# Kernel tuning notes

Measured on AMD Instinct MI355X. Metric: run time of the kernel, lower is better.

## Reference

```python
import jax, jax.numpy as jnp
import numpy as np

TAU_MIN, TAU_MAX = 5.0, 50.0
BOOST = 3.2
DECO_RATE = 0.01

B, I, F, Q = 4096, 1024, 2048, 4

def setup_inputs() -> dict:
    key = jax.random.key(0)
    ks = jax.random.split(key, 12)
    return {
        "inputs": jax.random.normal(ks[0], (B, I), jnp.float32),
        "hidden_state": jax.random.normal(ks[1], (B, F), jnp.float32),
        "W_in": jax.random.normal(ks[2], (I, F), jnp.float32) / np.sqrt(I),
        "b_in": jnp.zeros((F,), jnp.float32),
        "amp_real": jax.random.normal(ks[3], (F, Q), jnp.float32) * 0.1,
        "amp_imag": jax.random.normal(ks[4], (F, Q), jnp.float32) * 0.1,
        "phase": jax.random.uniform(ks[5], (F, Q), jnp.float32, 0.0, 2 * np.pi),
        "primary": jax.random.normal(ks[6], (F, F), jnp.float32) / np.sqrt(F),
        "ent_mat": jax.random.normal(ks[7], (F, F), jnp.float32) / np.sqrt(F),
        "corr": jax.random.uniform(ks[8], (F,), jnp.float32, 0.0, 0.7),
        "W_tau": jax.random.uniform(ks[9], (F, F), jnp.float32, 0.0, 0.1) / np.sqrt(F),
        "b_tau": jnp.zeros((F,), jnp.float32),
        "W_dec": jax.random.uniform(ks[10], (F, F), jnp.float32, 0.0, 0.5) / np.sqrt(F),
        "b_dec": jnp.zeros((F,), jnp.float32),
        "time_step": 1,
    }

def reference(inputs, hidden_state, W_in, b_in, amp_real, amp_imag, phase,
              primary, ent_mat, corr, W_tau, b_tau, W_dec, b_dec, time_step):
    t = jnp.float32(time_step)
    batch = inputs.shape[0]
    feats = hidden_state.shape[1]

    # input projection: [B,I] @ [I,F]
    x_proj = inputs @ W_in + b_in

    # quantum superposition state (batch-independent, [F,Q] params)
    ph = phase + t * 0.1
    real_c = amp_real * jnp.cos(ph)          # [F,Q]
    imag_c = amp_imag * jnp.sin(ph)          # [F,Q]
    sup_r = real_c.sum(-1)                    # [F]
    sup_i = imag_c.sum(-1)                    # [F]
    prob_amp = real_c ** 2 + imag_c ** 2      # [F,Q]
    q_state = sup_r * jnp.exp(-sup_i ** 2)    # [F]
    q_state_b = jnp.broadcast_to(q_state, (batch, feats))
    prob_amp_b = jnp.broadcast_to(prob_amp, (batch,) + prob_amp.shape)

    # entangled recurrent connections: two F x F matmuls
    ent_rec = hidden_state @ primary + (hidden_state @ ent_mat) * corr

    # quantum time constants
    tau_raw = q_state_b @ W_tau + b_tau
    tau_q = (TAU_MIN + (TAU_MAX - TAU_MIN) * jax.nn.sigmoid(tau_raw)) / BOOST

    # decoherence gate
    deco = jax.nn.sigmoid(q_state_b @ W_dec + b_dec)
    coherent = jnp.exp(-DECO_RATE * t)

    classical = jnp.tanh(x_proj + ent_rec)
    quantum_act = q_state_b * deco * coherent
    combined = classical + quantum_act

    dx_dt = (-hidden_state + combined) / tau_q
    dt_q = 0.1 / BOOST
    new_hidden = hidden_state + dt_q * dx_dt

    # diagnostics
    d_amp = jnp.mean(prob_amp_b, axis=-1)          # [B,F]
    d_coh = coherent
    d_ent = jnp.mean(jnp.abs(ent_rec))
    d_dec = jnp.mean(deco)
    d_tau = jnp.mean(tau_q)
    return (new_hidden, d_amp, d_coh, d_ent, d_dec, d_tau)
```

## Files before the change

kernel.cpp:

```cpp
#include <hip/hip_runtime.h>
#include <hip/hip_bf16.h>

#define BD 4096
#define ID 1024
#define FD 2048

typedef __bf16 v8bf __attribute__((ext_vector_type(8)));
typedef float  v4f  __attribute__((ext_vector_type(4)));

struct alignas(8) bf4 { __hip_bfloat16 x, y, z, w; };

__device__ inline __hip_bfloat16 bf(float f) { return __float2bfloat16(f); }
__device__ inline float sig(float x) { return 1.f / (1.f + expf(-x)); }

__device__ inline void gload16(const __hip_bfloat16* g, __hip_bfloat16* l) {
  __builtin_amdgcn_global_load_lds(
      (const __attribute__((address_space(1))) void*)g,
      (__attribute__((address_space(3))) void*)l, 16, 0, 0);
}

#define MB_CAST  12288
#define MB_PREP  (MB_CAST + 8)
#define MB_TCW   (MB_PREP + 2048)
#define MB_TCM   (MB_TCW + 4096)
#define MB_MV    (MB_TCM + 256)

__global__ void k_mega(
    const float* __restrict__ inputs, const float* __restrict__ hidden,
    const float* __restrict__ W_in, const float* __restrict__ primary,
    const float* __restrict__ ent_mat, const float* __restrict__ corr,
    const float* __restrict__ W_tau, const float* __restrict__ W_dec,
    const float* __restrict__ ar, const float* __restrict__ ai,
    const float* __restrict__ ph, const int* __restrict__ tstep,
    __hip_bfloat16* __restrict__ inputs_bf, __hip_bfloat16* __restrict__ hidden_bf,
    __hip_bfloat16* __restrict__ WT, __hip_bfloat16* __restrict__ MT,
    float* __restrict__ qs, float* __restrict__ pamp,
    float* __restrict__ ptau, float* __restrict__ pdec) {
  __shared__ float tbuf[32][33];
  __shared__ float q[128];
  const int b = blockIdx.x, tid = threadIdx.x;

  if (b < MB_CAST) {
    int i = b * 256 + tid;
    const float* src = inputs; __hip_bfloat16* dst = inputs_bf;
    int n1 = BD * ID / 4;
    if (i >= n1) { i -= n1; src = hidden; dst = hidden_bf; }
    float4 v = ((const float4*)src)[i];
    bf4 o{bf(v.x), bf(v.y), bf(v.z), bf(v.w)};
    ((bf4*)dst)[i] = o;

  } else if (b < MB_PREP) {
    int j = (b - MB_CAST) * 256 + tid;
    float t = (float)tstep[0];
    float4 a = ((const float4*)ar)[j];
    float4 bb = ((const float4*)ai)[j];
    float4 p = ((const float4*)ph)[j];
    float sr = 0.f, si = 0.f, pm = 0.f;
#pragma unroll
    for (int k = 0; k < 4; k++) {
      float pk = (&p.x)[k] + 0.1f * t;
      float rc = (&a.x)[k] * cosf(pk), ic = (&bb.x)[k] * sinf(pk);
      sr += rc; si += ic; pm += rc * rc + ic * ic;
    }
    qs[j] = sr * expf(-si * si);
    pamp[j] = 0.25f * pm;

  } else if (b < MB_TCM) {
    int isM = (b >= MB_TCW);
    int b2 = b - (isM ? MB_TCW : MB_PREP);
    const float* src = isM ? primary : W_in;
    const float* src2 = ent_mat;
    __hip_bfloat16* dst = isM ? MT : WT;
    int C = FD, R = isM ? FD : ID;
    int tx = tid & 31, ty = tid >> 5;
    int x = (b2 & 63) * 32 + tx;
    int yb = (b2 >> 6) * 32;
    float cr = isM ? corr[x] : 0.f;
#pragma unroll
    for (int j = 0; j < 4; j++) {
      int y = yb + ty + j * 8;
      float v = src[(size_t)y * C + x];
      if (isM) v += src2[(size_t)y * C + x] * cr;
      tbuf[ty + j * 8][tx] = v;
    }
    __syncthreads();
#pragma unroll
    for (int j = 0; j < 4; j++) {
      int orow = (b2 & 63) * 32 + ty + j * 8;
      int ocol = yb + tx;
      dst[(size_t)orow * R + ocol] = bf(tbuf[tx][ty + j * 8]);
    }

  } else {
    int b2 = b - MB_TCM;
    int jb = b2 & 7, p = (b2 >> 3) & 15, z = b2 >> 7;
    int i0 = p * 128;
    if (tid < 128) {
      int i = i0 + tid;
      float t = (float)tstep[0];
      float4 a = ((const float4*)ar)[i];
      float4 bb = ((const float4*)ai)[i];
      float4 pp = ((const float4*)ph)[i];
      float sr = 0.f, si = 0.f;
#pragma unroll
      for (int k = 0; k < 4; k++) {
        float pk = (&pp.x)[k] + 0.1f * t;
        sr += (&a.x)[k] * cosf(pk);
        si += (&bb.x)[k] * sinf(pk);
      }
      q[tid] = sr * expf(-si * si);
    }
    __syncthreads();
    const float* W = z ? W_dec : W_tau;
    float* outp = z ? pdec : ptau;
    int j = jb * 256 + tid;
    float acc = 0.f;
#pragma unroll 8
    for (int i = 0; i < 128; i++)
      acc = fmaf(q[i], W[(size_t)(i0 + i) * FD + j], acc);
    outp[p * FD + j] = acc;
  }
}

__global__ void k_post(const float* __restrict__ ptau, const float* __restrict__ pdec,
                       const float* __restrict__ qs, const float* __restrict__ b_tau,
                       const float* __restrict__ b_dec, const int* tstep,
                       float* __restrict__ s_arr, float* __restrict__ qact,
                       float* __restrict__ tpart, float* __restrict__ dpart) {
  int j = blockIdx.x * 256 + threadIdx.x;
  float tr = b_tau[j], dr = b_dec[j];
#pragma unroll
  for (int p = 0; p < 16; p++) {
    tr += ptau[p * FD + j];
    dr += pdec[p * FD + j];
  }
  float t = (float)tstep[0];
  float coh = expf(-0.01f * t);
  float tq = (5.f + 45.f * sig(tr)) / 3.2f;
  s_arr[j] = 0.03125f / tq;
  float dec = sig(dr);
  qact[j] = qs[j] * dec * coh;
  float tsum = tq, dsum = dec;
  for (int off = 32; off; off >>= 1) {
    tsum += __shfl_down(tsum, off);
    dsum += __shfl_down(dsum, off);
  }
  __shared__ float rt[4], rd[4];
  int w = threadIdx.x >> 6;
  if ((threadIdx.x & 63) == 0) { rt[w] = tsum; rd[w] = dsum; }
  __syncthreads();
  if (threadIdx.x == 0) {
    tpart[blockIdx.x] = rt[0] + rt[1] + rt[2] + rt[3];
    dpart[blockIdx.x] = rd[0] + rd[1] + rd[2] + rd[3];
  }
}

__global__ __launch_bounds__(256, 4) void k_gemm2(
    const __hip_bfloat16* __restrict__ Ah,
    const __hip_bfloat16* __restrict__ MT,
    const __hip_bfloat16* __restrict__ Ax,
    const __hip_bfloat16* __restrict__ WT,
    __hip_bfloat16* __restrict__ ge, __hip_bfloat16* __restrict__ gx) {
  __shared__ alignas(16) __hip_bfloat16 As[2][128][32];
  __shared__ alignas(16) __hip_bfloat16 Bs[2][128][32];

  const int tid = threadIdx.x;
  const int l = tid & 63, w = tid >> 6;
  const int wr = w >> 1, wc = w & 1;
  const int row0 = blockIdx.x * 128, col0 = blockIdx.y * 128;
  const int bz = blockIdx.z;

  const __hip_bfloat16* A = bz ? Ax : Ah;
  const __hip_bfloat16* B = bz ? WT : MT;
  const int ld = bz ? ID : FD;
  const int nkt = bz ? 32 : 64;
  __hip_bfloat16* gout = bz ? gx : ge;

  v4f acc[4][4];
#pragma unroll
  for (int i = 0; i < 4; i++)
#pragma unroll
    for (int j = 0; j < 4; j++) acc[i][j] = (v4f)0.f;

  const int srow = l >> 2;
  const int scol = ((l & 3) ^ ((l >> 3) & 3)) * 8;
  const int rcol = ((l >> 4) ^ ((l >> 1) & 3)) * 8;

  auto stage = [&](int buf, int kt) {
    int k = kt * 32;
#pragma unroll
    for (int i = 0; i < 2; i++) {
      int rr = w * 32 + i * 16;
      gload16(A + (size_t)(row0 + rr + srow) * ld + k + scol, &As[buf][rr][0]);
      gload16(B + (size_t)(col0 + rr + srow) * ld + k + scol, &Bs[buf][rr][0]);
    }
  };
  auto compute = [&](int buf) {
    v8bf a[4], b[4];
#pragma unroll
    for (int mi = 0; mi < 4; mi++)
      a[mi] = *(const v8bf*)&As[buf][wr * 64 + mi * 16 + (l & 15)][rcol];
#pragma unroll
    for (int ni = 0; ni < 4; ni++)
      b[ni] = *(const v8bf*)&Bs[buf][wc * 64 + ni * 16 + (l & 15)][rcol];
#pragma unroll
    for (int mi = 0; mi < 4; mi++)
#pragma unroll
      for (int ni = 0; ni < 4; ni++)
        acc[mi][ni] = __builtin_amdgcn_mfma_f32_16x16x32_bf16(a[mi], b[ni], acc[mi][ni], 0, 0, 0);
  };

  stage(0, 0);
  __syncthreads();
  for (int kt = 0; kt < nkt; kt++) {
    if (kt + 1 < nkt) stage((kt + 1) & 1, kt + 1);
    compute(kt & 1);
    __syncthreads();
  }

#pragma unroll
  for (int ni = 0; ni < 4; ni++) {
    int gc = col0 + wc * 64 + ni * 16 + (l & 15);
#pragma unroll
    for (int mi = 0; mi < 4; mi++) {
      int gr0 = row0 + wr * 64 + mi * 16 + (l >> 4) * 4;
#pragma unroll
      for (int e = 0; e < 4; e++)
        gout[(size_t)(gr0 + e) * FD + gc] = bf(acc[mi][ni][e]);
    }
  }
}

__global__ __launch_bounds__(256) void k_comb(
    const __hip_bfloat16* __restrict__ ge, const __hip_bfloat16* __restrict__ gx,
    const __hip_bfloat16* __restrict__ hbf,
    const float* __restrict__ b_in, const float* __restrict__ s_arr,
    const float* __restrict__ qact, const float* __restrict__ pamp,
    float* __restrict__ entpart, float* __restrict__ out) {
  const int row = blockIdx.x;
  const size_t rb = (size_t)row * FD;
  float asum = 0.f;
#pragma unroll
  for (int half = 0; half < 2; half++) {
    const int c = half * 1024 + threadIdx.x * 4;
    const size_t base = rb + c;
    bf4 e0 = *(const bf4*)(ge + base);
    bf4 xx = *(const bf4*)(gx + base);
    bf4 hh = *(const bf4*)(hbf + base);
    float4 bi = *(const float4*)&b_in[c];
    float4 sj = *(const float4*)&s_arr[c];
    float4 qa = *(const float4*)&qact[c];
    float4 pm = *(const float4*)&pamp[c];
    float o[4];
#pragma unroll
    for (int j = 0; j < 4; j++) {
      float e = __bfloat162float((&e0.x)[j]);
      asum += fabsf(e);
      float g = e + __bfloat162float((&xx.x)[j]) + (&bi.x)[j];
      float comb = tanhf(g) + (&qa.x)[j];
      float h = __bfloat162float((&hh.x)[j]);
      o[j] = fmaf((&sj.x)[j], comb - h, h);
    }
    *(float4*)&out[base] = make_float4(o[0], o[1], o[2], o[3]);
    *(float4*)&out[(size_t)BD * FD + base] = pm;
  }

  for (int off = 32; off; off >>= 1) asum += __shfl_down(asum, off);
  __shared__ float red[4];
  if ((threadIdx.x & 63) == 0) red[threadIdx.x >> 6] = asum;
  __syncthreads();
  if (threadIdx.x == 0)
    entpart[row] = red[0] + red[1] + red[2] + red[3];
}

__global__ void k_fin(const float* __restrict__ entpart, const float* __restrict__ tpart,
                      const float* __restrict__ dpart, const int* tstep, float* out3) {
  float s = 0.f;
  for (int i = threadIdx.x; i < BD; i += 256) s += entpart[i];
  for (int off = 32; off; off >>= 1) s += __shfl_down(s, off);
  __shared__ float red[4];
  if ((threadIdx.x & 63) == 0) red[threadIdx.x >> 6] = s;
  __syncthreads();
  if (threadIdx.x == 0) {
    float tot = red[0] + red[1] + red[2] + red[3];
    float ts = 0.f, ds = 0.f;
#pragma unroll
    for (int i = 0; i < 8; i++) { ts += tpart[i]; ds += dpart[i]; }
    float t = (float)tstep[0];
    out3[0] = expf(-0.01f * t);
    out3[1] = tot / (float)((size_t)BD * FD);
    out3[2] = ds / (float)FD;
    out3[3] = ts / (float)FD;
  }
}

extern "C" void kernel_launch(void* const* d_in, const int* in_sizes, int n_in,
                              void* d_out, int out_size, void* d_ws, size_t ws_size,
                              hipStream_t stream) {
  const float* inputs  = (const float*)d_in[0];
  const float* hidden  = (const float*)d_in[1];
  const float* W_in    = (const float*)d_in[2];
  const float* b_in    = (const float*)d_in[3];
  const float* amp_r   = (const float*)d_in[4];
  const float* amp_i   = (const float*)d_in[5];
  const float* phase   = (const float*)d_in[6];
  const float* primary = (const float*)d_in[7];
  const float* ent_mat = (const float*)d_in[8];
  const float* corr    = (const float*)d_in[9];
  const float* W_tau   = (const float*)d_in[10];
  const float* b_tau   = (const float*)d_in[11];
  const float* W_dec   = (const float*)d_in[12];
  const float* b_dec   = (const float*)d_in[13];
  const int*   tstep   = (const int*)d_in[14];

  char* ws = (char*)d_ws;
  __hip_bfloat16* inputs_bf = (__hip_bfloat16*)(ws + 0);
  __hip_bfloat16* hidden_bf = (__hip_bfloat16*)(ws + 8388608);
  __hip_bfloat16* WT        = (__hip_bfloat16*)(ws + 25165824);
  __hip_bfloat16* MT        = (__hip_bfloat16*)(ws + 29360128);
  __hip_bfloat16* ge        = (__hip_bfloat16*)(ws + 37748736);
  __hip_bfloat16* gx        = (__hip_bfloat16*)(ws + 54525952);

  char* sb = ws + 71303168;
  float* qs      = (float*)(sb);
  float* pamp    = (float*)(sb + 8192);
  float* s_arr   = (float*)(sb + 2 * 8192);
  float* qact    = (float*)(sb + 3 * 8192);
  float* ptau    = (float*)(sb + 4 * 8192);
  float* pdec    = (float*)(sb + 4 * 8192 + 131072);
  float* entpart = (float*)(sb + 4 * 8192 + 262144);
  float* tpart   = (float*)(sb + 4 * 8192 + 278528);
  float* dpart   = (float*)(sb + 4 * 8192 + 278528 + 64);

  float* out = (float*)d_out;

  hipLaunchKernelGGL(k_mega, dim3(MB_MV), dim3(256), 0, stream,
                     inputs, hidden, W_in, primary, ent_mat, corr, W_tau, W_dec,
                     amp_r, amp_i, phase, tstep,
                     inputs_bf, hidden_bf, WT, MT, qs, pamp, ptau, pdec);
  hipLaunchKernelGGL(k_post, dim3(8), dim3(256), 0, stream,
                     ptau, pdec, qs, b_tau, b_dec, tstep, s_arr, qact, tpart, dpart);
  hipLaunchKernelGGL(k_gemm2, dim3(32, 16, 2), dim3(256), 0, stream,
                     hidden_bf, MT, inputs_bf, WT, ge, gx);
  hipLaunchKernelGGL(k_comb, dim3(4096), dim3(256), 0, stream,
                     ge, gx, hidden_bf, b_in, s_arr, qact, pamp, entpart, out);
  hipLaunchKernelGGL(k_fin, dim3(1), dim3(256), 0, stream,
                     entpart, tpart, dpart, tstep, out + (size_t)2 * BD * FD);
}
```

Baseline: 125.8 us.

## Rebalance GEMM split-K across z-slices, fold k_post into GEMM launch, fast tanh

The hidden-state GEMM (K=2048) is split 48/16 k-tiles so that the z=1 blocks compute a partial hidden product plus the input projection (K=1024), evening out the work per block. A third partial buffer g2 is added and summed in the combine kernel. The small k_post kernel is folded into the GEMM launch as extra z=2 blocks, which removes one launch and its serialization. tanhf is replaced by an exp/rcp approximation. The costs are an extra bf16 intermediate write and read plus extra rounding, and many z=2 blocks launch only to exit immediately.

```diff
diff --git a/kernel.cpp b/kernel.cpp
--- a/kernel.cpp
+++ b/kernel.cpp
@@ -12,6 +12,10 @@
 
 __device__ inline __hip_bfloat16 bf(float f) { return __float2bfloat16(f); }
 __device__ inline float sig(float x) { return 1.f / (1.f + expf(-x)); }
+__device__ inline float tanh_fast(float x) {
+  float e = __expf(2.f * x);
+  return 1.f - 2.f * __builtin_amdgcn_rcpf(e + 1.f);
+}
 
 __device__ inline void gload16(const __hip_bfloat16* g, __hip_bfloat16* l) {
   __builtin_amdgcn_global_load_lds(
@@ -122,59 +126,57 @@
   }
 }
 
-__global__ void k_post(const float* __restrict__ ptau, const float* __restrict__ pdec,
-                       const float* __restrict__ qs, const float* __restrict__ b_tau,
-                       const float* __restrict__ b_dec, const int* tstep,
-                       float* __restrict__ s_arr, float* __restrict__ qact,
-                       float* __restrict__ tpart, float* __restrict__ dpart) {
-  int j = blockIdx.x * 256 + threadIdx.x;
-  float tr = b_tau[j], dr = b_dec[j];
-#pragma unroll
-  for (int p = 0; p < 16; p++) {
-    tr += ptau[p * FD + j];
-    dr += pdec[p * FD + j];
-  }
-  float t = (float)tstep[0];
-  float coh = expf(-0.01f * t);
-  float tq = (5.f + 45.f * sig(tr)) / 3.2f;
-  s_arr[j] = 0.03125f / tq;
-  float dec = sig(dr);
-  qact[j] = qs[j] * dec * coh;
-  float tsum = tq, dsum = dec;
-  for (int off = 32; off; off >>= 1) {
-    tsum += __shfl_down(tsum, off);
-    dsum += __shfl_down(dsum, off);
-  }
-  __shared__ float rt[4], rd[4];
-  int w = threadIdx.x >> 6;
-  if ((threadIdx.x & 63) == 0) { rt[w] = tsum; rd[w] = dsum; }
-  __syncthreads();
-  if (threadIdx.x == 0) {
-    tpart[blockIdx.x] = rt[0] + rt[1] + rt[2] + rt[3];
-    dpart[blockIdx.x] = rd[0] + rd[1] + rd[2] + rd[3];
-  }
-}
-
-__global__ __launch_bounds__(256, 4) void k_gemm2(
+__global__ __launch_bounds__(256, 4) void k_gemm3(
     const __hip_bfloat16* __restrict__ Ah,
     const __hip_bfloat16* __restrict__ MT,
     const __hip_bfloat16* __restrict__ Ax,
     const __hip_bfloat16* __restrict__ WT,
-    __hip_bfloat16* __restrict__ ge, __hip_bfloat16* __restrict__ gx) {
+    const float* __restrict__ ptau, const float* __restrict__ pdec,
+    const float* __restrict__ qs, const float* __restrict__ b_tau,
+    const float* __restrict__ b_dec, const int* __restrict__ tstep,
+    float* __restrict__ s_arr, float* __restrict__ qact,
+    float* __restrict__ tpart, float* __restrict__ dpart,
+    __hip_bfloat16* __restrict__ ge, __hip_bfloat16* __restrict__ g2,
+    __hip_bfloat16* __restrict__ gx) {
   __shared__ alignas(16) __hip_bfloat16 As[2][128][32];
   __shared__ alignas(16) __hip_bfloat16 Bs[2][128][32];
+  __shared__ float rt[4], rd[4];
 
   const int tid = threadIdx.x;
+
+  if (blockIdx.z == 2) {
+    if (blockIdx.x != 0 || blockIdx.y >= 8) return;
+    int j = blockIdx.y * 256 + tid;
+    float tr = b_tau[j], dr = b_dec[j];
+#pragma unroll
+    for (int p = 0; p < 16; p++) {
+      tr += ptau[p * FD + j];
+      dr += pdec[p * FD + j];
+    }
+    float t = (float)tstep[0];
+    float coh = expf(-0.01f * t);
+    float tq = (5.f + 45.f * sig(tr)) / 3.2f;
+    s_arr[j] = 0.03125f / tq;
+    float dec = sig(dr);
+    qact[j] = qs[j] * dec * coh;
+    float tsum = tq, dsum = dec;
+    for (int off = 32; off; off >>= 1) {
+      tsum += __shfl_down(tsum, off);
+      dsum += __shfl_down(dsum, off);
+    }
+    int w = tid >> 6;
+    if ((tid & 63) == 0) { rt[w] = tsum; rd[w] = dsum; }
+    __syncthreads();
+    if (tid == 0) {
+      tpart[blockIdx.y] = rt[0] + rt[1] + rt[2] + rt[3];
+      dpart[blockIdx.y] = rd[0] + rd[1] + rd[2] + rd[3];
+    }
+    return;
+  }
+
   const int l = tid & 63, w = tid >> 6;
   const int wr = w >> 1, wc = w & 1;
   const int row0 = blockIdx.x * 128, col0 = blockIdx.y * 128;
-  const int bz = blockIdx.z;
-
-  const __hip_bfloat16* A = bz ? Ax : Ah;
-  const __hip_bfloat16* B = bz ? WT : MT;
-  const int ld = bz ? ID : FD;
-  const int nkt = bz ? 32 : 64;
-  __hip_bfloat16* gout = bz ? gx : ge;
 
   v4f acc[4][4];
 #pragma unroll
@@ -186,8 +188,8 @@
   const int scol = ((l & 3) ^ ((l >> 3) & 3)) * 8;
   const int rcol = ((l >> 4) ^ ((l >> 1) & 3)) * 8;
 
-  auto stage = [&](int buf, int kt) {
-    int k = kt * 32;
+  auto stage = [&](int buf, const __hip_bfloat16* A, const __hip_bfloat16* B,
+                   int ld, int k) {
 #pragma unroll
     for (int i = 0; i < 2; i++) {
       int rr = w * 32 + i * 16;
@@ -209,31 +211,48 @@
       for (int ni = 0; ni < 4; ni++)
         acc[mi][ni] = __builtin_amdgcn_mfma_f32_16x16x32_bf16(a[mi], b[ni], acc[mi][ni], 0, 0, 0);
   };
-
-  stage(0, 0);
-  __syncthreads();
-  for (int kt = 0; kt < nkt; kt++) {
-    if (kt + 1 < nkt) stage((kt + 1) & 1, kt + 1);
-    compute(kt & 1);
+  auto run = [&](const __hip_bfloat16* A, const __hip_bfloat16* B, int ld,
+                 int kb, int nkt) {
+    stage(0, A, B, ld, kb);
     __syncthreads();
-  }
-
-#pragma unroll
-  for (int ni = 0; ni < 4; ni++) {
-    int gc = col0 + wc * 64 + ni * 16 + (l & 15);
-#pragma unroll
-    for (int mi = 0; mi < 4; mi++) {
-      int gr0 = row0 + wr * 64 + mi * 16 + (l >> 4) * 4;
-#pragma unroll
-      for (int e = 0; e < 4; e++)
-        gout[(size_t)(gr0 + e) * FD + gc] = bf(acc[mi][ni][e]);
-    }
+    for (int kt = 0; kt < nkt; kt++) {
+      if (kt + 1 < nkt) stage((kt + 1) & 1, A, B, ld, kb + (kt + 1) * 32);
+      compute(kt & 1);
+      __syncthreads();
+    }
+  };
+  auto writeout = [&](__hip_bfloat16* gout) {
+#pragma unroll
+    for (int ni = 0; ni < 4; ni++) {
+      int gc = col0 + wc * 64 + ni * 16 + (l & 15);
+#pragma unroll
+      for (int mi = 0; mi < 4; mi++) {
+        int gr0 = row0 + wr * 64 + mi * 16 + (l >> 4) * 4;
+#pragma unroll
+        for (int e = 0; e < 4; e++)
+          gout[(size_t)(gr0 + e) * FD + gc] = bf(acc[mi][ni][e]);
+      }
+    }
+  };
+
+  if (blockIdx.z == 0) {
+    run(Ah, MT, FD, 0, 48);
+    writeout(ge);
+  } else {
+    run(Ah, MT, FD, 1536, 16);
+    writeout(g2);
+#pragma unroll
+    for (int i = 0; i < 4; i++)
+#pragma unroll
+      for (int j = 0; j < 4; j++) acc[i][j] = (v4f)0.f;
+    run(Ax, WT, ID, 0, 32);
+    writeout(gx);
   }
 }
 
 __global__ __launch_bounds__(256) void k_comb(
-    const __hip_bfloat16* __restrict__ ge, const __hip_bfloat16* __restrict__ gx,
-    const __hip_bfloat16* __restrict__ hbf,
+    const __hip_bfloat16* __restrict__ ge, const __hip_bfloat16* __restrict__ g2,
+    const __hip_bfloat16* __restrict__ gx, const __hip_bfloat16* __restrict__ hbf,
     const float* __restrict__ b_in, const float* __restrict__ s_arr,
     const float* __restrict__ qact, const float* __restrict__ pamp,
     float* __restrict__ entpart, float* __restrict__ out) {
@@ -245,6 +264,7 @@
     const int c = half * 1024 + threadIdx.x * 4;
     const size_t base = rb + c;
     bf4 e0 = *(const bf4*)(ge + base);
+    bf4 e1 = *(const bf4*)(g2 + base);
     bf4 xx = *(const bf4*)(gx + base);
     bf4 hh = *(const bf4*)(hbf + base);
     float4 bi = *(const float4*)&b_in[c];
@@ -254,10 +274,10 @@
     float o[4];
 #pragma unroll
     for (int j = 0; j < 4; j++) {
-      float e = __bfloat162float((&e0.x)[j]);
+      float e = __bfloat162float((&e0.x)[j]) + __bfloat162float((&e1.x)[j]);
       asum += fabsf(e);
       float g = e + __bfloat162float((&xx.x)[j]) + (&bi.x)[j];
-      float comb = tanhf(g) + (&qa.x)[j];
+      float comb = tanh_fast(g) + (&qa.x)[j];
       float h = __bfloat162float((&hh.x)[j]);
       o[j] = fmaf((&sj.x)[j], comb - h, h);
     }
@@ -320,8 +340,9 @@
   __hip_bfloat16* MT        = (__hip_bfloat16*)(ws + 29360128);
   __hip_bfloat16* ge        = (__hip_bfloat16*)(ws + 37748736);
   __hip_bfloat16* gx        = (__hip_bfloat16*)(ws + 54525952);
-
-  char* sb = ws + 71303168;
+  __hip_bfloat16* g2        = (__hip_bfloat16*)(ws + 71303168);
+
+  char* sb = ws + 88080384;
   float* qs      = (float*)(sb);
   float* pamp    = (float*)(sb + 8192);
   float* s_arr   = (float*)(sb + 2 * 8192);
@@ -329,8 +350,8 @@
   float* ptau    = (float*)(sb + 4 * 8192);
   float* pdec    = (float*)(sb + 4 * 8192 + 131072);
   float* entpart = (float*)(sb + 4 * 8192 + 262144);
-  float* tpart   = (float*)(sb + 4 * 8192 + 278528);
-  float* dpart   = (float*)(sb + 4 * 8192 + 278528 + 64);
+  float* tpart   = (float*)(sb + 4 * 8192 + 262144 + 16384);
+  float* dpart   = (float*)(sb + 4 * 8192 + 262144 + 16384 + 64);
 
   float* out = (float*)d_out;
 
@@ -338,12 +359,13 @@
                      inputs, hidden, W_in, primary, ent_mat, corr, W_tau, W_dec,
                      amp_r, amp_i, phase, tstep,
                      inputs_bf, hidden_bf, WT, MT, qs, pamp, ptau, pdec);
-  hipLaunchKernelGGL(k_post, dim3(8), dim3(256), 0, stream,
-                     ptau, pdec, qs, b_tau, b_dec, tstep, s_arr, qact, tpart, dpart);
-  hipLaunchKernelGGL(k_gemm2, dim3(32, 16, 2), dim3(256), 0, stream,
-                     hidden_bf, MT, inputs_bf, WT, ge, gx);
-  hipLaunchKernelGGL(k_comb, dim3(4096), dim3(256), 0, stream,
-                     ge, gx, hidden_bf, b_in, s_arr, qact, pamp, entpart, out);
+  hipLaunchKernelGGL(k_gemm3, dim3(32, 16, 3), dim3(256), 0, stream,
+                     hidden_bf, MT, inputs_bf, WT,
+                     ptau, pdec, qs, b_tau, b_dec, tstep,
+                     s_arr, qact, tpart, dpart, ge, g2, gx);
+  hipLaunchKernelGGL(k_comb, dim3(BD), dim3(256), 0, stream,
+                     ge, g2, gx, hidden_bf, b_in, s_arr, qact, pamp,
+                     entpart, out);
   hipLaunchKernelGGL(k_fin, dim3(1), dim3(256), 0, stream,
                      entpart, tpart, dpart, tstep, out + (size_t)2 * BD * FD);
 }
```

Result: slower. 146.0 us (+16.1%).
